# Kernel optimization log

Measured on AMD Instinct MI355X. Metric: run time of the kernel, lower is better.

The kernel has to match this reference:

```python
import jax, jax.numpy as jnp
import numpy as np

N = 50000      # nodes
E = 800000     # edges (before self-loops)
HD = 256       # hidden_dim
H = 4          # heads
C = 64         # per-head channels (hidden_dim // 4)
L = 3          # num_layers
G = 512        # graphs in batch
NEG = 0.2      # LeakyReLU negative slope
EPS = 1e-5     # BatchNorm eps


def setup_inputs() -> dict:
    key = jax.random.key(0)
    ks = jax.random.split(key, 16)
    s_in = 1.0 / np.sqrt(HD)
    inp = {
        "x": jax.random.normal(ks[0], (N, 9), dtype=jnp.float32),
        "edge_index": jax.random.randint(ks[1], (2, E), 0, N, dtype=jnp.int64),
        "edge_attr": jax.random.normal(ks[2], (E, 5), dtype=jnp.float32),
        "batch": jnp.sort(jax.random.randint(ks[3], (N,), 0, G, dtype=jnp.int64)),
        # embeddings
        "Wn": jax.random.normal(ks[4], (9, HD), dtype=jnp.float32) / 3.0,
        "bn_b": jnp.zeros((HD,), jnp.float32),
        "We": jax.random.normal(ks[5], (5, HD), dtype=jnp.float32) / 2.3,
        "be_b": jnp.zeros((HD,), jnp.float32),
        # per-layer GATConv params (stacked over L)
        "lin_w": jax.random.normal(ks[6], (L, HD, H * C), dtype=jnp.float32) * s_in,
        "att_src": jax.random.normal(ks[7], (L, H, C), dtype=jnp.float32) * s_in,
        "att_dst": jax.random.normal(ks[8], (L, H, C), dtype=jnp.float32) * s_in,
        "lin_edge_w": jax.random.normal(ks[9], (L, HD, H * C), dtype=jnp.float32) * s_in,
        "att_edge": jax.random.normal(ks[10], (L, H, C), dtype=jnp.float32) * s_in,
        "conv_bias": jnp.zeros((L, H * C), jnp.float32),
        # BatchNorm affine params (eval mode: running_mean=0, running_var=1)
        "gamma": jnp.ones((L, HD), jnp.float32),
        "beta": jnp.zeros((L, HD), jnp.float32),
    }
    return inp


def _segment_softmax(logits, seg, num):
    m = jax.ops.segment_max(logits, seg, num_segments=num)
    m = jnp.where(jnp.isfinite(m), m, 0.0)
    e = jnp.exp(logits - m[seg])
    s = jax.ops.segment_sum(e, seg, num_segments=num)
    return e / (s[seg] + 1e-16)


def _gat_layer(x, row, col, edge_attr, lin_w, att_s, att_d, lin_e_w, att_e, bias):
    # add self-loops; self-loop edge_attr = mean of incoming edge_attr (PyG fill_value='mean')
    deg = jax.ops.segment_sum(jnp.ones((row.shape[0],), x.dtype), col, num_segments=N)
    loop_attr = jax.ops.segment_sum(edge_attr, col, num_segments=N) / jnp.maximum(deg, 1.0)[:, None]
    sl = jnp.arange(N, dtype=row.dtype)
    r = jnp.concatenate([row, sl])
    c = jnp.concatenate([col, sl])
    ea = jnp.concatenate([edge_attr, loop_attr], axis=0)  # [E+N, HD]

    xh = (x @ lin_w).reshape(N, H, C)                     # [N,H,C]
    a_src = jnp.einsum('nhc,hc->nh', xh, att_s)           # [N,H]
    a_dst = jnp.einsum('nhc,hc->nh', xh, att_d)
    eh = (ea @ lin_e_w).reshape(-1, H, C)                 # [E+N,H,C]
    a_e = jnp.einsum('ehc,hc->eh', eh, att_e)

    alpha = a_src[r] + a_dst[c] + a_e                     # [E+N,H]
    alpha = jnp.where(alpha >= 0, alpha, NEG * alpha)     # leaky_relu
    alpha = _segment_softmax(alpha, c, N)

    msg = xh[r] * alpha[:, :, None]                       # gather + weight
    out = jax.ops.segment_sum(msg, c, num_segments=N)     # scatter-add
    return out.reshape(N, H * C) + bias


def reference(x, edge_index, edge_attr, batch, Wn, bn_b, We, be_b,
              lin_w, att_src, att_dst, lin_edge_w, att_edge, conv_bias,
              gamma, beta):
    row, col = edge_index[0], edge_index[1]
    h = x @ Wn + bn_b                     # node embedding [N,HD]
    ea = edge_attr @ We + be_b            # edge embedding [E,HD]
    inv_std = 1.0 / jnp.sqrt(1.0 + EPS)   # BN eval, running stats (0,1)
    for l in range(L):
        h = _gat_layer(h, row, col, ea, lin_w[l], att_src[l], att_dst[l],
                       lin_edge_w[l], att_edge[l], conv_bias[l])
        h = h * inv_std * gamma[l] + beta[l]
        h = jax.nn.relu(h)                # dropout = identity (eval)
    # global mean pool over graphs
    cnt = jax.ops.segment_sum(jnp.ones((N,), h.dtype), batch, num_segments=G)
    pooled = jax.ops.segment_sum(h, batch, num_segments=G) / jnp.maximum(cnt, 1.0)[:, None]
    return pooled
```

## Files before the change

### kernel.cpp

```cpp
#include <hip/hip_runtime.h>
#include <hip/hip_fp16.h>
#include <math.h>

#define HD 256
#define NHEAD 4
#define CH 64
#define NLAYER 3
#define NEG_SLOPE 0.2f

typedef __attribute__((ext_vector_type(8))) _Float16 half8;
typedef __attribute__((ext_vector_type(4))) _Float16 half4v;
typedef __attribute__((ext_vector_type(4))) float float4v;

__global__ __launch_bounds__(256) void node_embed_kernel(
    const float* __restrict__ x, const float* __restrict__ Wn,
    const float* __restrict__ bn_b, float* __restrict__ h, int N) {
  int n = blockIdx.x;
  int c = threadIdx.x;
  __shared__ float xs[9];
  if (c < 9) xs[c] = x[(size_t)n * 9 + c];
  __syncthreads();
  float v = bn_b[c];
#pragma unroll
  for (int k = 0; k < 9; ++k) v += xs[k] * Wn[k * HD + c];
  h[(size_t)n * HD + c] = v;
}

__global__ __launch_bounds__(256) void precompute_wc_kernel(
    const float* __restrict__ lin_edge_w, const float* __restrict__ att_edge,
    const float* __restrict__ We, const float* __restrict__ be_b,
    float* __restrict__ Wc, float* __restrict__ bc) {
  int lh = blockIdx.x;
  int l = lh >> 2, hh = lh & 3;
  __shared__ float weff[256];
  int j = threadIdx.x;
  const float* lw = lin_edge_w + (size_t)l * HD * HD + (size_t)j * HD + hh * CH;
  const float* ae = att_edge + l * HD + hh * CH;
  float s = 0.f;
#pragma unroll 8
  for (int c = 0; c < CH; ++c) s += lw[c] * ae[c];
  weff[j] = s;
  __syncthreads();
  if (j < 5) {
    float acc = 0.f;
    for (int t = 0; t < 256; ++t) acc += We[j * HD + t] * weff[t];
    Wc[j * 12 + lh] = acc;
  } else if (j == 5) {
    float acc = 0.f;
    for (int t = 0; t < 256; ++t) acc += be_b[t] * weff[t];
    bc[lh] = acc;
  }
}

__global__ __launch_bounds__(64) void conv_bfrag_kernel(
    const float* __restrict__ lin_w, _Float16* __restrict__ Bf_hi) {
  int bid = blockIdx.x;
  int l = bid >> 7;
  int kt = (bid >> 4) & 7, nt = bid & 15;
  int lane = threadIdx.x;
  const float* B = lin_w + (size_t)l * HD * HD;
  size_t base = ((size_t)bid * 64 + lane) * 8;
  int k0 = kt * 32 + (lane >> 4) * 8;
  int n = (lane & 15) * 16 + nt;
#pragma unroll
  for (int j = 0; j < 8; ++j) {
    Bf_hi[base + j] = (_Float16)B[(size_t)(k0 + j) * HD + n];
  }
}

__global__ __launch_bounds__(256) void count_deg_kernel(
    const int* __restrict__ col, int* __restrict__ deg, int E) {
  int e = blockIdx.x * 256 + threadIdx.x;
  if (e < E) atomicAdd(&deg[col[e]], 1);
}

__global__ __launch_bounds__(256) void tile_sums_kernel(
    const int* __restrict__ deg, int* __restrict__ tsum, int N) {
  __shared__ int red[256];
  int i = blockIdx.x * 256 + threadIdx.x;
  red[threadIdx.x] = (i < N) ? deg[i] : 0;
  __syncthreads();
  for (int off = 128; off > 0; off >>= 1) {
    if (threadIdx.x < off) red[threadIdx.x] += red[threadIdx.x + off];
    __syncthreads();
  }
  if (threadIdx.x == 0) tsum[blockIdx.x] = red[0];
}

__global__ __launch_bounds__(64) void scan_tsums_kernel(
    const int* __restrict__ tsum, int* __restrict__ toff, int T) {
  int lane = threadIdx.x;
  int carry = 0;
  for (int base = 0; base < T; base += 64) {
    int i = base + lane;
    int orig = (i < T) ? tsum[i] : 0;
    int v = orig;
#pragma unroll
    for (int off = 1; off < 64; off <<= 1) {
      int t = __shfl_up(v, off, 64);
      if (lane >= off) v += t;
    }
    if (i < T) toff[i] = carry + v - orig;
    carry += __shfl(v, 63, 64);
  }
}

__global__ __launch_bounds__(256) void scan_local_kernel(
    const int* __restrict__ deg, const int* __restrict__ toff,
    int* __restrict__ row_start, int N, int E) {
  __shared__ int buf[256];
  int i = blockIdx.x * 256 + threadIdx.x;
  int v = (i < N) ? deg[i] : 0;
  buf[threadIdx.x] = v;
  __syncthreads();
  for (int off = 1; off < 256; off <<= 1) {
    int t = (threadIdx.x >= off) ? buf[threadIdx.x - off] : 0;
    __syncthreads();
    buf[threadIdx.x] += t;
    __syncthreads();
  }
  if (i < N) row_start[i] = toff[blockIdx.x] + buf[threadIdx.x] - v;
  if (blockIdx.x == 0 && threadIdx.x == 0) row_start[N] = E;
}

__global__ __launch_bounds__(256) void scatter_csr_ae_kernel(
    const int* __restrict__ row, const int* __restrict__ col,
    const float* __restrict__ edge_attr, const int* __restrict__ row_start,
    int* __restrict__ cursor, int* __restrict__ rowc,
    const float* __restrict__ Wc, const float* __restrict__ bc,
    float* __restrict__ ae4c_all, int E) {
  __shared__ float sWc[60];
  __shared__ float sbc[12];
  int t = threadIdx.x;
  if (t < 60) sWc[t] = Wc[t];
  if (t < 12) sbc[t] = bc[t];
  __syncthreads();
  int e = blockIdx.x * 256 + t;
  if (e >= E) return;
  int c = col[e];
  int p = atomicAdd(&cursor[c], 1);
  int slot = row_start[c] + p;
  rowc[slot] = row[e];
  float ea[5];
#pragma unroll
  for (int k = 0; k < 5; ++k) ea[k] = edge_attr[(size_t)e * 5 + k];
#pragma unroll
  for (int l = 0; l < NLAYER; ++l) {
    float av[NHEAD];
#pragma unroll
    for (int hh = 0; hh < NHEAD; ++hh) {
      int lh = l * NHEAD + hh;
      float s = sbc[lh];
#pragma unroll
      for (int k = 0; k < 5; ++k) s += ea[k] * sWc[k * 12 + lh];
      av[hh] = s;
    }
    *(float4*)(ae4c_all + ((size_t)l * E + slot) * 4) =
        make_float4(av[0], av[1], av[2], av[3]);
  }
}

__global__ __launch_bounds__(512) void mfma_gemm_fused_kernel(
    const float* __restrict__ A, const _Float16* __restrict__ Bf_hi,
    const float* __restrict__ att_s, const float* __restrict__ att_d,
    __half* __restrict__ xh_h, float* __restrict__ a_src,
    float* __restrict__ a_dst, int N) {
  __shared__ _Float16 sBh[8192];
  const int tid = threadIdx.x;
  const int wave = tid >> 6, lane = tid & 63;
  const int m = lane & 15, quad = lane >> 4;
  const int rowbase = blockIdx.x * 128 + wave * 16;
  const int arow = rowbase + m;
  const int arowc = (arow < N) ? arow : (N - 1);

  float4v acc[16];
#pragma unroll
  for (int nt = 0; nt < 16; ++nt) acc[nt] = (float4v){0.f, 0.f, 0.f, 0.f};

  for (int kt = 0; kt < 8; ++kt) {
    __syncthreads();
    {
      const float4* gh = (const float4*)(Bf_hi + (size_t)kt * 8192);
      float4* dh = (float4*)sBh;
      dh[tid] = gh[tid];
      dh[tid + 512] = gh[tid + 512];
    }
    const float* ap = A + (size_t)arowc * HD + kt * 32 + quad * 8;
    float4 av0 = *(const float4*)(ap);
    float4 av1 = *(const float4*)(ap + 4);
    float af[8] = {av0.x, av0.y, av0.z, av0.w, av1.x, av1.y, av1.z, av1.w};
    half8 ahi, alo;
#pragma unroll
    for (int j = 0; j < 8; ++j) {
      _Float16 hi = (_Float16)af[j];
      ahi[j] = hi;
      alo[j] = (_Float16)(af[j] - (float)hi);
    }
    __syncthreads();
#pragma unroll
    for (int nt = 0; nt < 16; ++nt) {
      half8 bhi = *(const half8*)&sBh[nt * 512 + lane * 8];
      acc[nt] = __builtin_amdgcn_mfma_f32_16x16x32_f16(ahi, bhi, acc[nt], 0, 0, 0);
      acc[nt] = __builtin_amdgcn_mfma_f32_16x16x32_f16(alo, bhi, acc[nt], 0, 0, 0);
    }
  }

  const int hh = m >> 2;
  float ats[16], atd[16];
#pragma unroll
  for (int nt = 0; nt < 16; ++nt) {
    ats[nt] = att_s[m * 16 + nt];
    atd[nt] = att_d[m * 16 + nt];
  }
  _Float16* xf = (_Float16*)xh_h;
#pragma unroll
  for (int r = 0; r < 4; ++r) {
    int orow = rowbase + quad * 4 + r;
    bool valid = orow < N;
    float ps = 0.f, pd = 0.f;
    half8 h0, h1;
#pragma unroll
    for (int nt = 0; nt < 8; ++nt) {
      h0[nt] = (_Float16)acc[nt][r];
      h1[nt] = (_Float16)acc[nt + 8][r];
      ps += acc[nt][r] * ats[nt] + acc[nt + 8][r] * ats[nt + 8];
      pd += acc[nt][r] * atd[nt] + acc[nt + 8][r] * atd[nt + 8];
    }
    if (valid) {
      _Float16* dst = xf + (size_t)orow * HD + m * 16;
      *(half8*)dst = h0;
      *(half8*)(dst + 8) = h1;
    }
    ps += __shfl_xor(ps, 1, 64);
    ps += __shfl_xor(ps, 2, 64);
    pd += __shfl_xor(pd, 1, 64);
    pd += __shfl_xor(pd, 2, 64);
    if (valid && (m & 3) == 0) {
      a_src[(size_t)orow * NHEAD + hh] = ps;
      a_dst[(size_t)orow * NHEAD + hh] = pd;
    }
  }
}

__global__ __launch_bounds__(256) void fused_aggregate_kernel(
    const __half* __restrict__ xh_h, const int* __restrict__ rowc,
    const int* __restrict__ row_start, const float* __restrict__ ae4c_l,
    const float* __restrict__ a_src, const float* __restrict__ a_dst,
    const float* __restrict__ cb, const float* __restrict__ gm,
    const float* __restrict__ bt, float inv_std, float* __restrict__ hout,
    int N) {
  int tid = threadIdx.x;
  int n = blockIdx.x * 4 + (tid >> 6);
  if (n >= N) return;
  int lane = tid & 63;
  int s = row_start[n], e = row_start[n + 1];

  int hh1 = lane & 3, j = lane >> 2;
  float based1 = a_dst[n * 4 + hh1];
  float m = -3e38f, ssum = 0.f, aes = 0.f;
  for (int i = s + j; i < e; i += 16) {
    int r = rowc[i];
    float ae = ae4c_l[(size_t)i * 4 + hh1];
    float lg = a_src[r * 4 + hh1] + based1 + ae;
    lg = (lg >= 0.f) ? lg : NEG_SLOPE * lg;
    aes += ae;
    float mn = fmaxf(m, lg);
    ssum = ssum * __expf(m - mn) + __expf(lg - mn);
    m = mn;
  }
#pragma unroll
  for (int off = 4; off < 64; off <<= 1) {
    float m2 = __shfl_xor(m, off, 64);
    float s2 = __shfl_xor(ssum, off, 64);
    aes += __shfl_xor(aes, off, 64);
    float mn = fmaxf(m, m2);
    ssum = ssum * __expf(m - mn) + s2 * __expf(m2 - mn);
    m = mn;
  }
  float dinv = (e > s) ? 1.0f / (float)(e - s) : 1.0f;
  float sl = a_src[n * 4 + hh1] + based1 + aes * dinv;
  sl = (sl >= 0.f) ? sl : NEG_SLOPE * sl;
  float mfin = fmaxf(m, sl);
  float self_e = __expf(sl - mfin);
  float tot = ssum * __expf(m - mfin) + self_e;
  float is = 1.0f / (tot + 1e-16f);
  float selfw = self_e * is;

  int hw = lane >> 4;
  float m_h = __shfl(mfin, hw, 64);
  float is_h = __shfl(is, hw, 64);
  float sw_h = __shfl(selfw, hw, 64);
  float based2 = a_dst[n * 4 + hw];

  int eidx = lane & 15;
  int t = lane;
  int ch = t * 4;
  const half4v* xh4 = (const half4v*)xh_h;

  half4v sv = xh4[(size_t)n * 64 + t];
  float a0 = sw_h * (float)sv[0], a1 = sw_h * (float)sv[1];
  float a2 = sw_h * (float)sv[2], a3 = sw_h * (float)sv[3];

  const int base_src = lane & 48;
  for (int chunk = s; chunk < e; chunk += 16) {
    int myedge = chunk + eidx;
    int r_my = 0;
    float w_my = 0.f;
    if (myedge < e) {
      r_my = rowc[myedge];
      float lg = a_src[r_my * 4 + hw] + based2 + ae4c_l[(size_t)myedge * 4 + hw];
      lg = (lg >= 0.f) ? lg : NEG_SLOPE * lg;
      w_my = __expf(lg - m_h) * is_h;
    }
#pragma unroll
    for (int u = 0; u < 16; ++u) {
      float w = __shfl(w_my, base_src + u, 64);
      int ru = __shfl(r_my, base_src + u, 64);
      half4v xv = xh4[(size_t)ru * 64 + t];
      a0 += w * (float)xv[0];
      a1 += w * (float)xv[1];
      a2 += w * (float)xv[2];
      a3 += w * (float)xv[3];
    }
  }
  float4 outv;
  outv.x = fmaxf((a0 + cb[ch + 0]) * inv_std * gm[ch + 0] + bt[ch + 0], 0.f);
  outv.y = fmaxf((a1 + cb[ch + 1]) * inv_std * gm[ch + 1] + bt[ch + 1], 0.f);
  outv.z = fmaxf((a2 + cb[ch + 2]) * inv_std * gm[ch + 2] + bt[ch + 2], 0.f);
  outv.w = fmaxf((a3 + cb[ch + 3]) * inv_std * gm[ch + 3] + bt[ch + 3], 0.f);
  *(float4*)&hout[(size_t)n * HD + ch] = outv;
}

__global__ __launch_bounds__(128) void pool_kernel(
    const float* __restrict__ h, const int* __restrict__ batch,
    float* __restrict__ out, int N) {
  int g = blockIdx.x;
  int ch = blockIdx.y * 128 + threadIdx.x;
  __shared__ int s_lo, s_hi;
  if (threadIdx.x == 0) {
    int lo = 0, hi = N;
    while (lo < hi) { int mid = (lo + hi) >> 1; if (batch[mid] < g) lo = mid + 1; else hi = mid; }
    s_lo = lo;
    lo = 0; hi = N;
    while (lo < hi) { int mid = (lo + hi) >> 1; if (batch[mid] < g + 1) lo = mid + 1; else hi = mid; }
    s_hi = lo;
  }
  __syncthreads();
  int lo = s_lo, hi = s_hi;
  float acc = 0.f;
  for (int n = lo; n < hi; ++n) acc += h[(size_t)n * HD + ch];
  int cnt = hi - lo;
  out[(size_t)g * HD + ch] = acc / (float)(cnt > 0 ? cnt : 1);
}

extern "C" void kernel_launch(void* const* d_in, const int* in_sizes, int n_in,
                              void* d_out, int out_size, void* d_ws, size_t ws_size,
                              hipStream_t stream) {
  const float* x = (const float*)d_in[0];
  const int* ei = (const int*)d_in[1];
  const float* edge_attr = (const float*)d_in[2];
  const int* batch = (const int*)d_in[3];
  const float* Wn = (const float*)d_in[4];
  const float* bn_b = (const float*)d_in[5];
  const float* We = (const float*)d_in[6];
  const float* be_b = (const float*)d_in[7];
  const float* lin_w = (const float*)d_in[8];
  const float* att_src = (const float*)d_in[9];
  const float* att_dst = (const float*)d_in[10];
  const float* lin_edge_w = (const float*)d_in[11];
  const float* att_edge = (const float*)d_in[12];
  const float* conv_bias = (const float*)d_in[13];
  const float* gamma = (const float*)d_in[14];
  const float* beta = (const float*)d_in[15];

  const int N = in_sizes[3];
  const int E = in_sizes[1] / 2;
  const int G = out_size / HD;
  const int* row = ei;
  const int* col = ei + E;

  char* ws = (char*)d_ws;
  size_t off = 0;
  auto alloc = [&](size_t bytes) -> char* {
    char* p = ws + off;
    off += (bytes + 255) & ~(size_t)255;
    return p;
  };
  float* h = (float*)alloc((size_t)N * HD * 4);
  __half* xh_h = (__half*)alloc((size_t)N * HD * 2);
  float* a_src = (float*)alloc((size_t)N * NHEAD * 4);
  float* a_dst = (float*)alloc((size_t)N * NHEAD * 4);
  float* ae4c_all = (float*)alloc((size_t)NLAYER * E * NHEAD * 4);
  int* deg = (int*)alloc((size_t)N * 4);
  int* row_start = (int*)alloc((size_t)(N + 1) * 4);
  int* cursor = (int*)alloc((size_t)N * 4);
  int* rowc = (int*)alloc((size_t)E * 4);
  int* tsum = (int*)alloc(4096);
  int* toff = (int*)alloc(4096);
  float* Wc = (float*)alloc(64 * 4);
  float* bc = (float*)alloc(16 * 4);
  _Float16* Bf_hi = (_Float16*)alloc((size_t)NLAYER * HD * HD * 2);

  hipMemsetAsync(deg, 0, (size_t)N * 4, stream);
  hipMemsetAsync(cursor, 0, (size_t)N * 4, stream);

  node_embed_kernel<<<N, 256, 0, stream>>>(x, Wn, bn_b, h, N);
  precompute_wc_kernel<<<12, 256, 0, stream>>>(lin_edge_w, att_edge, We, be_b, Wc, bc);
  conv_bfrag_kernel<<<NLAYER * 128, 64, 0, stream>>>(lin_w, Bf_hi);
  count_deg_kernel<<<(E + 255) / 256, 256, 0, stream>>>(col, deg, E);
  int T = (N + 255) / 256;
  tile_sums_kernel<<<T, 256, 0, stream>>>(deg, tsum, N);
  scan_tsums_kernel<<<1, 64, 0, stream>>>(tsum, toff, T);
  scan_local_kernel<<<T, 256, 0, stream>>>(deg, toff, row_start, N, E);
  scatter_csr_ae_kernel<<<(E + 255) / 256, 256, 0, stream>>>(
      row, col, edge_attr, row_start, cursor, rowc, Wc, bc, ae4c_all, E);

  const float inv_std = 1.0f / sqrtf(1.0f + 1e-5f);
  for (int l = 0; l < NLAYER; ++l) {
    mfma_gemm_fused_kernel<<<(N + 127) / 128, 512, 0, stream>>>(
        h, Bf_hi + (size_t)l * HD * HD,
        att_src + l * HD, att_dst + l * HD, xh_h, a_src, a_dst, N);
    fused_aggregate_kernel<<<(N + 3) / 4, 256, 0, stream>>>(
        xh_h, rowc, row_start, ae4c_all + (size_t)l * E * NHEAD, a_src, a_dst,
        conv_bias + l * HD, gamma + l * HD, beta + l * HD, inv_std, h, N);
  }
  dim3 pg(G, 2);
  pool_kernel<<<pg, 128, 0, stream>>>(h, batch, (float*)d_out, N);
}
```

Baseline: 574.7 us.

## Split GEMM output columns across two blocks and batch node embedding rows

```diff
diff --git a/kernel.cpp b/kernel.cpp
--- a/kernel.cpp
+++ b/kernel.cpp
@@ -15,15 +15,20 @@
 __global__ __launch_bounds__(256) void node_embed_kernel(
     const float* __restrict__ x, const float* __restrict__ Wn,
     const float* __restrict__ bn_b, float* __restrict__ h, int N) {
-  int n = blockIdx.x;
+  int base = blockIdx.x * 8;
   int c = threadIdx.x;
-  __shared__ float xs[9];
-  if (c < 9) xs[c] = x[(size_t)n * 9 + c];
-  __syncthreads();
-  float v = bn_b[c];
-#pragma unroll
-  for (int k = 0; k < 9; ++k) v += xs[k] * Wn[k * HD + c];
-  h[(size_t)n * HD + c] = v;
+  __shared__ float xs[8][9];
+  int nn = N - base;
+  if (nn > 8) nn = 8;
+  if (c < nn * 9) xs[c / 9][c % 9] = x[(size_t)base * 9 + c];
+  __syncthreads();
+  float b = bn_b[c];
+  for (int i = 0; i < nn; ++i) {
+    float v = b;
+#pragma unroll
+    for (int k = 0; k < 9; ++k) v += xs[i][k] * Wn[k * HD + c];
+    h[(size_t)(base + i) * HD + c] = v;
+  }
 }
 
 __global__ __launch_bounds__(256) void precompute_wc_kernel(
@@ -56,12 +61,12 @@
     const float* __restrict__ lin_w, _Float16* __restrict__ Bf_hi) {
   int bid = blockIdx.x;
   int l = bid >> 7;
-  int kt = (bid >> 4) & 7, nt = bid & 15;
+  int kt = (bid >> 4) & 7, ntg = bid & 15;
   int lane = threadIdx.x;
   const float* B = lin_w + (size_t)l * HD * HD;
   size_t base = ((size_t)bid * 64 + lane) * 8;
   int k0 = kt * 32 + (lane >> 4) * 8;
-  int n = (lane & 15) * 16 + nt;
+  int n = ((ntg >= 8) ? 128 : 0) + (lane & 15) * 8 + (ntg & 7);
 #pragma unroll
   for (int j = 0; j < 8; ++j) {
     Bf_hi[base + j] = (_Float16)B[(size_t)(k0 + j) * HD + n];
@@ -165,25 +170,24 @@
     const float* __restrict__ att_s, const float* __restrict__ att_d,
     __half* __restrict__ xh_h, float* __restrict__ a_src,
     float* __restrict__ a_dst, int N) {
-  __shared__ _Float16 sBh[8192];
+  __shared__ _Float16 sBh[4096];
   const int tid = threadIdx.x;
   const int wave = tid >> 6, lane = tid & 63;
   const int m = lane & 15, quad = lane >> 4;
+  const int y = blockIdx.y;
   const int rowbase = blockIdx.x * 128 + wave * 16;
   const int arow = rowbase + m;
   const int arowc = (arow < N) ? arow : (N - 1);
 
-  float4v acc[16];
-#pragma unroll
-  for (int nt = 0; nt < 16; ++nt) acc[nt] = (float4v){0.f, 0.f, 0.f, 0.f};
+  float4v acc[8];
+#pragma unroll
+  for (int nt = 0; nt < 8; ++nt) acc[nt] = (float4v){0.f, 0.f, 0.f, 0.f};
 
   for (int kt = 0; kt < 8; ++kt) {
     __syncthreads();
     {
-      const float4* gh = (const float4*)(Bf_hi + (size_t)kt * 8192);
-      float4* dh = (float4*)sBh;
-      dh[tid] = gh[tid];
-      dh[tid + 512] = gh[tid + 512];
+      const float4* gh = (const float4*)(Bf_hi + ((size_t)kt * 16 + y * 8) * 512);
+      ((float4*)sBh)[tid] = gh[tid];
     }
     const float* ap = A + (size_t)arowc * HD + kt * 32 + quad * 8;
     float4 av0 = *(const float4*)(ap);
@@ -198,19 +202,20 @@
     }
     __syncthreads();
 #pragma unroll
-    for (int nt = 0; nt < 16; ++nt) {
+    for (int nt = 0; nt < 8; ++nt) {
       half8 bhi = *(const half8*)&sBh[nt * 512 + lane * 8];
       acc[nt] = __builtin_amdgcn_mfma_f32_16x16x32_f16(ahi, bhi, acc[nt], 0, 0, 0);
       acc[nt] = __builtin_amdgcn_mfma_f32_16x16x32_f16(alo, bhi, acc[nt], 0, 0, 0);
     }
   }
 
-  const int hh = m >> 2;
-  float ats[16], atd[16];
-#pragma unroll
-  for (int nt = 0; nt < 16; ++nt) {
-    ats[nt] = att_s[m * 16 + nt];
-    atd[nt] = att_d[m * 16 + nt];
+  const int hh = y * 2 + (m >> 3);
+  const int colbase = y * 128 + m * 8;
+  float ats[8], atd[8];
+#pragma unroll
+  for (int nt = 0; nt < 8; ++nt) {
+    ats[nt] = att_s[colbase + nt];
+    atd[nt] = att_d[colbase + nt];
   }
   _Float16* xf = (_Float16*)xh_h;
 #pragma unroll
@@ -218,24 +223,23 @@
     int orow = rowbase + quad * 4 + r;
     bool valid = orow < N;
     float ps = 0.f, pd = 0.f;
-    half8 h0, h1;
+    half8 h0;
 #pragma unroll
     for (int nt = 0; nt < 8; ++nt) {
       h0[nt] = (_Float16)acc[nt][r];
-      h1[nt] = (_Float16)acc[nt + 8][r];
-      ps += acc[nt][r] * ats[nt] + acc[nt + 8][r] * ats[nt + 8];
-      pd += acc[nt][r] * atd[nt] + acc[nt + 8][r] * atd[nt + 8];
+      ps += acc[nt][r] * ats[nt];
+      pd += acc[nt][r] * atd[nt];
     }
     if (valid) {
-      _Float16* dst = xf + (size_t)orow * HD + m * 16;
-      *(half8*)dst = h0;
-      *(half8*)(dst + 8) = h1;
+      *(half8*)(xf + (size_t)orow * HD + colbase) = h0;
     }
     ps += __shfl_xor(ps, 1, 64);
     ps += __shfl_xor(ps, 2, 64);
+    ps += __shfl_xor(ps, 4, 64);
     pd += __shfl_xor(pd, 1, 64);
     pd += __shfl_xor(pd, 2, 64);
-    if (valid && (m & 3) == 0) {
+    pd += __shfl_xor(pd, 4, 64);
+    if (valid && (m & 7) == 0) {
       a_src[(size_t)orow * NHEAD + hh] = ps;
       a_dst[(size_t)orow * NHEAD + hh] = pd;
     }
@@ -404,7 +408,7 @@
   hipMemsetAsync(deg, 0, (size_t)N * 4, stream);
   hipMemsetAsync(cursor, 0, (size_t)N * 4, stream);
 
-  node_embed_kernel<<<N, 256, 0, stream>>>(x, Wn, bn_b, h, N);
+  node_embed_kernel<<<(N + 7) / 8, 256, 0, stream>>>(x, Wn, bn_b, h, N);
   precompute_wc_kernel<<<12, 256, 0, stream>>>(lin_edge_w, att_edge, We, be_b, Wc, bc);
   conv_bfrag_kernel<<<NLAYER * 128, 64, 0, stream>>>(lin_w, Bf_hi);
   count_deg_kernel<<<(E + 255) / 256, 256, 0, stream>>>(col, deg, E);
@@ -417,7 +421,8 @@
 
   const float inv_std = 1.0f / sqrtf(1.0f + 1e-5f);
   for (int l = 0; l < NLAYER; ++l) {
-    mfma_gemm_fused_kernel<<<(N + 127) / 128, 512, 0, stream>>>(
+    dim3 gg((N + 127) / 128, 2);
+    mfma_gemm_fused_kernel<<<gg, 512, 0, stream>>>(
         h, Bf_hi + (size_t)l * HD * HD,
         att_src + l * HD, att_dst + l * HD, xh_h, a_src, a_dst, N);
     fused_aggregate_kernel<<<(N + 3) / 4, 256, 0, stream>>>(
```

Result: faster. 558.5 us (-2.8%).
